# Kernel tuning notes

Measured on AMD Instinct MI355X. Metric: run time of the kernel, lower is better.

## Reference

```python
import jax, jax.numpy as jnp
import numpy as np

H = 50  # hidden size
I = 1   # input size


def setup_inputs() -> dict:
    key = jax.random.key(0)
    ks = jax.random.split(key, 7)
    B, T = 4096, 512
    s = 1.0 / np.sqrt(H)  # PyTorch default init scale
    x = jax.random.normal(ks[0], (B, T, I), dtype=jnp.float32)
    W_ih = jax.random.uniform(ks[1], (4 * H, I), jnp.float32, -s, s)
    W_hh = jax.random.uniform(ks[2], (4 * H, H), jnp.float32, -s, s)
    b_ih = jax.random.uniform(ks[3], (4 * H,), jnp.float32, -s, s)
    b_hh = jax.random.uniform(ks[4], (4 * H,), jnp.float32, -s, s)
    W_out = jax.random.uniform(ks[5], (1, H), jnp.float32, -s, s)
    b_out = jax.random.uniform(ks[6], (1,), jnp.float32, -s, s)
    return {"x": x, "W_ih": W_ih, "W_hh": W_hh, "b_ih": b_ih,
            "b_hh": b_hh, "W_out": W_out, "b_out": b_out}


def _lstm(x, W_ih, W_hh, b_ih, b_hh):
    # x: [B, T, I]; gate order in PyTorch: i, f, g, o
    B = x.shape[0]
    b = b_ih + b_hh
    # precompute input projection for all timesteps: [T, B, 4H]
    xg = jnp.einsum('bti,gi->tbg', x, W_ih) + b

    def step(carry, xg_t):
        h, c = carry
        gates = xg_t + h @ W_hh.T  # [B, 4H]
        i, f, g, o = jnp.split(gates, 4, axis=-1)
        c = jax.nn.sigmoid(f) * c + jax.nn.sigmoid(i) * jnp.tanh(g)
        h = jax.nn.sigmoid(o) * jnp.tanh(c)
        return (h, c), h

    h0 = jnp.zeros((B, H), x.dtype)
    c0 = jnp.zeros((B, H), x.dtype)
    _, hs = jax.lax.scan(step, (h0, c0), xg)  # hs: [T, B, H]
    return hs.transpose(1, 0, 2)  # [B, T, H]


def reference(x, W_ih, W_hh, b_ih, b_hh, W_out, b_out):
    h = _lstm(x, W_ih, W_hh, b_ih, b_hh)          # [B, T, H]
    return h @ W_out.T + b_out                     # [B, T, 1]
```

## Files before the change

kernel.cpp:

```cpp
#include <hip/hip_runtime.h>
#include <math.h>

#define HID 50
#define TT  512
#define BT  16
#define NCW 13
#define NTH 896
#define HS  72
#define L2E 1.44269504088896f
#define K2C 2.88539008177793f

typedef __attribute__((ext_vector_type(8))) short bf16x8;
typedef __attribute__((ext_vector_type(4))) float f32x4;

__device__ __forceinline__ unsigned short bf16_rtne(float f) {
    unsigned u = __float_as_uint(f);
    u = (u + 0x7FFFu + ((u >> 16) & 1u)) >> 16;
    return (unsigned short)u;
}
__device__ __forceinline__ float bf16_f32(unsigned short s) {
    return __uint_as_float(((unsigned)s) << 16);
}

__global__ __launch_bounds__(NTH, 1) void lstm_mfma16_kernel(
    const float* __restrict__ x,
    const float* __restrict__ W_ih,
    const float* __restrict__ W_hh,
    const float* __restrict__ b_ih,
    const float* __restrict__ b_hh,
    const float* __restrict__ W_out,
    const float* __restrict__ b_out,
    float* __restrict__ out)
{
    const int tid  = threadIdx.x;
    const int lane = tid & 63;
    const int wv   = tid >> 6;
    const int col  = lane & 15;
    const int quad = lane >> 4;

    __shared__ __align__(16) unsigned short Hh[2][BT][HS];

    for (int i = tid; i < 2 * BT * HS; i += NTH)
        (&Hh[0][0][0])[i] = 0;

    bf16x8 Ah[2];
    float cs = 0.f;
    const int uo  = wv * 4 + quad;
    const int uo2 = (uo < HID) ? uo : uo + 5;

    if (wv < NCW) {
        const int gh  = wv * 16 + col;
        const int u   = gh >> 2;
        const int ty  = gh & 3;
        const bool vl = (u < HID);
        const int og  = ty * HID + u;
        const float sc = (ty == 2) ? K2C : L2E;
        #pragma unroll
        for (int kk = 0; kk < 2; ++kk) {
            #pragma unroll
            for (int j = 0; j < 8; ++j) {
                const int k = kk * 32 + quad * 8 + j;
                float v = 0.f;
                if (vl) {
                    if (k < HID)      v = sc * W_hh[og * HID + k];
                    else if (k == 50) v = sc * W_ih[og];
                    else if (k == 51) v = sc * (b_ih[og] + b_hh[og]);
                    else if (k == 52) v = sc * W_ih[og];
                    else if (k == 53) {
                        const float sb = sc * (b_ih[og] + b_hh[og]);
                        v = sb - bf16_f32(bf16_rtne(sb));
                    } else if (k == 54) {
                        const float sw = sc * W_ih[og];
                        v = sw - bf16_f32(bf16_rtne(sw));
                    }
                }
                Ah[kk][j] = (short)bf16_rtne(v);
            }
        }
    } else {
        #pragma unroll
        for (int kk = 0; kk < 2; ++kk) {
            #pragma unroll
            for (int j = 0; j < 8; ++j) {
                const int k = kk * 32 + quad * 8 + j;
                const float v = (k < HID) ? W_out[k] : 0.f;
                const unsigned short hi = bf16_rtne(v);
                short val = 0;
                if (col == 0)      val = (short)hi;
                else if (col == 1) val = (short)bf16_rtne(v - bf16_f32(hi));
                Ah[kk][j] = val;
            }
        }
    }
    const float bo = b_out[0];
    float* yout = out + (size_t)blockIdx.x * BT * TT + (size_t)(lane & 15) * TT;

    const int xb = (lane >= 16) ? (lane - 16) : 0;
    const float* xrow = x + (size_t)(blockIdx.x * BT + xb) * TT;
    float xa = 0.f;
    if (wv == NCW && lane >= 16 && lane < 32)
        xa = xrow[1];

    __syncthreads();

    if (tid < BT) {
        const float x0 = x[(size_t)(blockIdx.x * BT + tid) * TT];
        const unsigned short hx = bf16_rtne(x0);
        const unsigned short lx = bf16_rtne(x0 - bf16_f32(hx));
        unsigned* row32 = (unsigned*)&Hh[0][tid][0];
        row32[25] = (unsigned)hx | (0x3F80u << 16);
        row32[26] = (unsigned)lx | (0x3F80u << 16);
        Hh[0][tid][54] = hx;
    }
    __syncthreads();

    const unsigned short* rdA = &Hh[0][col][quad * 8];
    const unsigned short* rdB = &Hh[1][col][quad * 8];
    unsigned short* wrA = &Hh[1][col][uo2];
    unsigned short* wrB = &Hh[0][col][uo2];
    unsigned* xwA = (unsigned*)&Hh[1][xb][0];
    unsigned* xwB = (unsigned*)&Hh[0][xb][0];
    const f32x4 z = {0.f, 0.f, 0.f, 0.f};

#define LSTM_STEP(RD, WR, XW, TI)                                             \
    do {                                                                      \
        if (wv < NCW) {                                                       \
            const bf16x8 B0 = *(const bf16x8*)(RD);                           \
            const bf16x8 B1 = *(const bf16x8*)((RD) + 32);                    \
            f32x4 a0 = __builtin_amdgcn_mfma_f32_16x16x32_bf16(Ah[0], B0, z, 0, 0, 0); \
            a0 = __builtin_amdgcn_mfma_f32_16x16x32_bf16(Ah[1], B1, a0, 0, 0, 0); \
            const float Ei = __builtin_amdgcn_exp2f(-a0.x);                   \
            const float Ef = __builtin_amdgcn_exp2f(-a0.y);                   \
            const float Eg = __builtin_amdgcn_exp2f(a0.z);                    \
            const float Eo = __builtin_amdgcn_exp2f(-a0.w);                   \
            const float DIG = (1.f + Ei) * (1.f + Eg);                        \
            const float DF  = 1.f + Ef;                                       \
            const float t1  = fmaf(K2C, Eg, -K2C);                            \
            const float num = fmaf(cs, DIG, t1 * DF);                         \
            cs = num * __builtin_amdgcn_rcpf(DF * DIG);                       \
            const float Ec = __builtin_amdgcn_exp2f(cs);                      \
            const float h  = (Ec - 1.f) *                                     \
                             __builtin_amdgcn_rcpf((1.f + Eo) * (1.f + Ec));  \
            unsigned hpk;                                                     \
            asm("v_cvt_pk_bf16_f32 %0, %1, %2" : "=v"(hpk) : "v"(h), "v"(h)); \
            *(WR) = (unsigned short)hpk;                                      \
        } else {                                                              \
            const bf16x8 B0 = *(const bf16x8*)(RD);                           \
            const bf16x8 B1 = *(const bf16x8*)((RD) + 32);                    \
            if (lane >= 16 && lane < 32) {                                    \
                const unsigned short hx = bf16_rtne(xa);                      \
                const unsigned short lx = bf16_rtne(xa - bf16_f32(hx));       \
                (XW)[25] = (unsigned)hx | (0x3F80u << 16);                    \
                (XW)[26] = (unsigned)lx | (0x3F80u << 16);                    \
                ((unsigned short*)(XW))[54] = hx;                             \
                xa = xrow[((TI) + 2 < TT) ? (TI) + 2 : TT - 1];               \
            }                                                                 \
            f32x4 a0 = __builtin_amdgcn_mfma_f32_16x16x32_bf16(Ah[0], B0, z, 0, 0, 0); \
            a0 = __builtin_amdgcn_mfma_f32_16x16x32_bf16(Ah[1], B1, a0, 0, 0, 0); \
            if (lane < 16 && (TI) > 0)                                        \
                yout[(TI) - 1] = a0.x + a0.y + bo;                            \
        }                                                                     \
    } while (0)

    for (int t = 0; t < TT; t += 2) {
        LSTM_STEP(rdA, wrA, xwA, t);
        asm volatile("s_waitcnt lgkmcnt(0)\n\ts_barrier" ::: "memory");
        LSTM_STEP(rdB, wrB, xwB, t + 1);
        asm volatile("s_waitcnt lgkmcnt(0)\n\ts_barrier" ::: "memory");
    }
#undef LSTM_STEP

    if (wv == NCW) {
        const bf16x8 B0 = *(const bf16x8*)rdA;
        const bf16x8 B1 = *(const bf16x8*)(rdA + 32);
        f32x4 a0 = __builtin_amdgcn_mfma_f32_16x16x32_bf16(Ah[0], B0, z, 0, 0, 0);
        a0 = __builtin_amdgcn_mfma_f32_16x16x32_bf16(Ah[1], B1, a0, 0, 0, 0);
        if (lane < 16)
            yout[TT - 1] = a0.x + a0.y + bo;
    }
}

extern "C" void kernel_launch(void* const* d_in, const int* in_sizes, int n_in,
                              void* d_out, int out_size, void* d_ws, size_t ws_size,
                              hipStream_t stream) {
    const float* x     = (const float*)d_in[0];
    const float* W_ih  = (const float*)d_in[1];
    const float* W_hh  = (const float*)d_in[2];
    const float* b_ih  = (const float*)d_in[3];
    const float* b_hh  = (const float*)d_in[4];
    const float* W_out = (const float*)d_in[5];
    const float* b_out = (const float*)d_in[6];
    float* out = (float*)d_out;

    const int B = in_sizes[0] / TT;
    lstm_mfma16_kernel<<<B / BT, NTH, 0, stream>>>(x, W_ih, W_hh, b_ih, b_hh,
                                                   W_out, b_out, out);
}
```

Measured before the change: 241.1 us.

## Give each compute wave two gate tiles, shrinking block to 8 waves

Each compute wavefront now owns two 16-row gate tiles, issuing four interleaved MFMAs and two gate evaluations per step. The block shrinks from 14 to 8 waves, so the per-step barrier synchronises fewer waves and the two packed h values share one bf16 convert. The cost is a longer serial chain of MFMA and transcendental work per wave on the recurrence's critical path, plus more registers. The padded 14th tile (units 52-55) is still handled through the uo+5 remap.

```diff
diff --git a/kernel.cpp b/kernel.cpp
--- a/kernel.cpp
+++ b/kernel.cpp
@@ -4,8 +4,8 @@
 #define HID 50
 #define TT  512
 #define BT  16
-#define NCW 13
-#define NTH 896
+#define NCW 7
+#define NTH 512
 #define HS  72
 #define L2E 1.44269504088896f
 #define K2C 2.88539008177793f
@@ -22,7 +22,7 @@
     return __uint_as_float(((unsigned)s) << 16);
 }
 
-__global__ __launch_bounds__(NTH, 1) void lstm_mfma16_kernel(
+__global__ __launch_bounds__(NTH, 1) void lstm_mfma17_kernel(
     const float* __restrict__ x,
     const float* __restrict__ W_ih,
     const float* __restrict__ W_hh,
@@ -43,38 +43,43 @@
     for (int i = tid; i < 2 * BT * HS; i += NTH)
         (&Hh[0][0][0])[i] = 0;
 
-    bf16x8 Ah[2];
-    float cs = 0.f;
-    const int uo  = wv * 4 + quad;
-    const int uo2 = (uo < HID) ? uo : uo + 5;
+    bf16x8 Ah[2][2];
+    float cs0 = 0.f, cs1 = 0.f;
+    const int uoa = (wv * 2) * 4 + quad;
+    const int uob = (wv * 2 + 1) * 4 + quad;
+    const int uo2a = (uoa < HID) ? uoa : uoa + 5;
+    const int uo2b = (uob < HID) ? uob : uob + 5;
 
     if (wv < NCW) {
-        const int gh  = wv * 16 + col;
-        const int u   = gh >> 2;
-        const int ty  = gh & 3;
-        const bool vl = (u < HID);
-        const int og  = ty * HID + u;
-        const float sc = (ty == 2) ? K2C : L2E;
         #pragma unroll
-        for (int kk = 0; kk < 2; ++kk) {
+        for (int i = 0; i < 2; ++i) {
+            const int gh  = (wv * 2 + i) * 16 + col;
+            const int u   = gh >> 2;
+            const int ty  = gh & 3;
+            const bool vl = (u < HID);
+            const int og  = ty * HID + u;
+            const float sc = (ty == 2) ? K2C : L2E;
             #pragma unroll
-            for (int j = 0; j < 8; ++j) {
-                const int k = kk * 32 + quad * 8 + j;
-                float v = 0.f;
-                if (vl) {
-                    if (k < HID)      v = sc * W_hh[og * HID + k];
-                    else if (k == 50) v = sc * W_ih[og];
-                    else if (k == 51) v = sc * (b_ih[og] + b_hh[og]);
-                    else if (k == 52) v = sc * W_ih[og];
-                    else if (k == 53) {
-                        const float sb = sc * (b_ih[og] + b_hh[og]);
-                        v = sb - bf16_f32(bf16_rtne(sb));
-                    } else if (k == 54) {
-                        const float sw = sc * W_ih[og];
-                        v = sw - bf16_f32(bf16_rtne(sw));
+            for (int kk = 0; kk < 2; ++kk) {
+                #pragma unroll
+                for (int j = 0; j < 8; ++j) {
+                    const int k = kk * 32 + quad * 8 + j;
+                    float v = 0.f;
+                    if (vl) {
+                        if (k < HID)      v = sc * W_hh[og * HID + k];
+                        else if (k == 50) v = sc * W_ih[og];
+                        else if (k == 51) v = sc * (b_ih[og] + b_hh[og]);
+                        else if (k == 52) v = sc * W_ih[og];
+                        else if (k == 53) {
+                            const float sb = sc * (b_ih[og] + b_hh[og]);
+                            v = sb - bf16_f32(bf16_rtne(sb));
+                        } else if (k == 54) {
+                            const float sw = sc * W_ih[og];
+                            v = sw - bf16_f32(bf16_rtne(sw));
+                        }
                     }
+                    Ah[i][kk][j] = (short)bf16_rtne(v);
                 }
-                Ah[kk][j] = (short)bf16_rtne(v);
             }
         }
     } else {
@@ -88,7 +93,8 @@
                 short val = 0;
                 if (col == 0)      val = (short)hi;
                 else if (col == 1) val = (short)bf16_rtne(v - bf16_f32(hi));
-                Ah[kk][j] = val;
+                Ah[0][kk][j] = val;
+                Ah[1][kk][j] = 0;
             }
         }
     }
@@ -116,34 +122,46 @@
 
     const unsigned short* rdA = &Hh[0][col][quad * 8];
     const unsigned short* rdB = &Hh[1][col][quad * 8];
-    unsigned short* wrA = &Hh[1][col][uo2];
-    unsigned short* wrB = &Hh[0][col][uo2];
+    unsigned short* wrA0 = &Hh[1][col][uo2a];
+    unsigned short* wrA1 = &Hh[1][col][uo2b];
+    unsigned short* wrB0 = &Hh[0][col][uo2a];
+    unsigned short* wrB1 = &Hh[0][col][uo2b];
     unsigned* xwA = (unsigned*)&Hh[1][xb][0];
     unsigned* xwB = (unsigned*)&Hh[0][xb][0];
     const f32x4 z = {0.f, 0.f, 0.f, 0.f};
 
-#define LSTM_STEP(RD, WR, XW, TI)                                             \
+#define GATES(ACC, CS, HOUT)                                                  \
+    do {                                                                      \
+        const float Ei = __builtin_amdgcn_exp2f(-(ACC).x);                    \
+        const float Ef = __builtin_amdgcn_exp2f(-(ACC).y);                    \
+        const float Eg = __builtin_amdgcn_exp2f((ACC).z);                     \
+        const float Eo = __builtin_amdgcn_exp2f(-(ACC).w);                    \
+        const float DIG = (1.f + Ei) * (1.f + Eg);                            \
+        const float DF  = 1.f + Ef;                                           \
+        const float t1  = fmaf(K2C, Eg, -K2C);                                \
+        const float num = fmaf((CS), DIG, t1 * DF);                           \
+        (CS) = num * __builtin_amdgcn_rcpf(DF * DIG);                         \
+        const float Ec = __builtin_amdgcn_exp2f(CS);                          \
+        (HOUT) = (Ec - 1.f) *                                                 \
+                 __builtin_amdgcn_rcpf((1.f + Eo) * (1.f + Ec));              \
+    } while (0)
+
+#define LSTM_STEP(RD, WR0, WR1, XW, TI)                                       \
     do {                                                                      \
         if (wv < NCW) {                                                       \
             const bf16x8 B0 = *(const bf16x8*)(RD);                           \
             const bf16x8 B1 = *(const bf16x8*)((RD) + 32);                    \
-            f32x4 a0 = __builtin_amdgcn_mfma_f32_16x16x32_bf16(Ah[0], B0, z, 0, 0, 0); \
-            a0 = __builtin_amdgcn_mfma_f32_16x16x32_bf16(Ah[1], B1, a0, 0, 0, 0); \
-            const float Ei = __builtin_amdgcn_exp2f(-a0.x);                   \
-            const float Ef = __builtin_amdgcn_exp2f(-a0.y);                   \
-            const float Eg = __builtin_amdgcn_exp2f(a0.z);                    \
-            const float Eo = __builtin_amdgcn_exp2f(-a0.w);                   \
-            const float DIG = (1.f + Ei) * (1.f + Eg);                        \
-            const float DF  = 1.f + Ef;                                       \
-            const float t1  = fmaf(K2C, Eg, -K2C);                            \
-            const float num = fmaf(cs, DIG, t1 * DF);                         \
-            cs = num * __builtin_amdgcn_rcpf(DF * DIG);                       \
-            const float Ec = __builtin_amdgcn_exp2f(cs);                      \
-            const float h  = (Ec - 1.f) *                                     \
-                             __builtin_amdgcn_rcpf((1.f + Eo) * (1.f + Ec));  \
+            f32x4 a0 = __builtin_amdgcn_mfma_f32_16x16x32_bf16(Ah[0][0], B0, z, 0, 0, 0); \
+            f32x4 a1 = __builtin_amdgcn_mfma_f32_16x16x32_bf16(Ah[1][0], B0, z, 0, 0, 0); \
+            a0 = __builtin_amdgcn_mfma_f32_16x16x32_bf16(Ah[0][1], B1, a0, 0, 0, 0); \
+            a1 = __builtin_amdgcn_mfma_f32_16x16x32_bf16(Ah[1][1], B1, a1, 0, 0, 0); \
+            float h0, h1;                                                     \
+            GATES(a0, cs0, h0);                                               \
+            GATES(a1, cs1, h1);                                               \
             unsigned hpk;                                                     \
-            asm("v_cvt_pk_bf16_f32 %0, %1, %2" : "=v"(hpk) : "v"(h), "v"(h)); \
-            *(WR) = (unsigned short)hpk;                                      \
+            asm("v_cvt_pk_bf16_f32 %0, %1, %2" : "=v"(hpk) : "v"(h0), "v"(h1)); \
+            *(WR0) = (unsigned short)(hpk & 0xFFFFu);                         \
+            *(WR1) = (unsigned short)(hpk >> 16);                             \
         } else {                                                              \
             const bf16x8 B0 = *(const bf16x8*)(RD);                           \
             const bf16x8 B1 = *(const bf16x8*)((RD) + 32);                    \
@@ -155,26 +173,27 @@
                 ((unsigned short*)(XW))[54] = hx;                             \
                 xa = xrow[((TI) + 2 < TT) ? (TI) + 2 : TT - 1];               \
             }                                                                 \
-            f32x4 a0 = __builtin_amdgcn_mfma_f32_16x16x32_bf16(Ah[0], B0, z, 0, 0, 0); \
-            a0 = __builtin_amdgcn_mfma_f32_16x16x32_bf16(Ah[1], B1, a0, 0, 0, 0); \
+            f32x4 a0 = __builtin_amdgcn_mfma_f32_16x16x32_bf16(Ah[0][0], B0, z, 0, 0, 0); \
+            a0 = __builtin_amdgcn_mfma_f32_16x16x32_bf16(Ah[0][1], B1, a0, 0, 0, 0); \
             if (lane < 16 && (TI) > 0)                                        \
                 yout[(TI) - 1] = a0.x + a0.y + bo;                            \
         }                                                                     \
     } while (0)
 
     for (int t = 0; t < TT; t += 2) {
-        LSTM_STEP(rdA, wrA, xwA, t);
+        LSTM_STEP(rdA, wrA0, wrA1, xwA, t);
         asm volatile("s_waitcnt lgkmcnt(0)\n\ts_barrier" ::: "memory");
-        LSTM_STEP(rdB, wrB, xwB, t + 1);
+        LSTM_STEP(rdB, wrB0, wrB1, xwB, t + 1);
         asm volatile("s_waitcnt lgkmcnt(0)\n\ts_barrier" ::: "memory");
     }
 #undef LSTM_STEP
+#undef GATES
 
     if (wv == NCW) {
         const bf16x8 B0 = *(const bf16x8*)rdA;
         const bf16x8 B1 = *(const bf16x8*)(rdA + 32);
-        f32x4 a0 = __builtin_amdgcn_mfma_f32_16x16x32_bf16(Ah[0], B0, z, 0, 0, 0);
-        a0 = __builtin_amdgcn_mfma_f32_16x16x32_bf16(Ah[1], B1, a0, 0, 0, 0);
+        f32x4 a0 = __builtin_amdgcn_mfma_f32_16x16x32_bf16(Ah[0][0], B0, z, 0, 0, 0);
+        a0 = __builtin_amdgcn_mfma_f32_16x16x32_bf16(Ah[0][1], B1, a0, 0, 0, 0);
         if (lane < 16)
             yout[TT - 1] = a0.x + a0.y + bo;
     }
@@ -193,6 +212,6 @@
     float* out = (float*)d_out;
 
     const int B = in_sizes[0] / TT;
-    lstm_mfma16_kernel<<<B / BT, NTH, 0, stream>>>(x, W_ih, W_hh, b_ih, b_hh,
+    lstm_mfma17_kernel<<<B / BT, NTH, 0, stream>>>(x, W_ih, W_hh, b_ih, b_hh,
                                                    W_out, b_out, out);
 }
```

Result: faster. 232.0 us (-3.8%).
